# Kernel optimization log

Hardware: AMD Instinct MI355X
Metric: run time of the kernel (lower is better)

Reference implementation:

```python
import jax, jax.numpy as jnp
import numpy as np

N_LAYERS = 200
KSIZE = 7
L_IN = 1388
FC_IN = 188   # 1388 - 200*6
FC_OUT = 91


def setup_inputs() -> dict:
    key = jax.random.key(0)
    k_x, k_w, k_b, k_fw, k_fb = jax.random.split(key, 5)
    B = 1024
    x = jax.random.normal(k_x, (B, L_IN), dtype=jnp.float32)
    # Conv1d(1,1,7) weights: torch default init U(-s, s) with s = 1/sqrt(in_ch*k) = 1/sqrt(7)
    s = 1.0 / np.sqrt(KSIZE)
    conv_w = jax.random.uniform(k_w, (N_LAYERS, KSIZE), dtype=jnp.float32, minval=-s, maxval=s)
    conv_b = jax.random.uniform(k_b, (N_LAYERS,), dtype=jnp.float32, minval=-s, maxval=s)
    sf = 1.0 / np.sqrt(FC_IN)
    fc_w = jax.random.uniform(k_fw, (FC_OUT, FC_IN), dtype=jnp.float32, minval=-sf, maxval=sf)
    fc_b = jax.random.uniform(k_fb, (FC_OUT,), dtype=jnp.float32, minval=-sf, maxval=sf)
    return {"x": x, "conv_w": conv_w, "conv_b": conv_b, "fc_w": fc_w, "fc_b": fc_b}


def _conv1(h, w, b):
    # h: [B, L]; cross-correlation with taps w[0..6], valid padding -> [B, L-6]
    L_out = h.shape[1] - (KSIZE - 1)
    acc = w[0] * h[:, 0:L_out]
    for k in range(1, KSIZE):
        acc = acc + w[k] * h[:, k:k + L_out]
    return acc + b


def reference(x, conv_w, conv_b, fc_w, fc_b):
    h = x  # unsqueeze(1) is implicit: single channel handled as [B, L]
    for i in range(N_LAYERS):
        h = _conv1(h, conv_w[i], conv_b[i])
        if i < N_LAYERS - 1:  # last ReLU was popped in the torch module
            h = jax.nn.relu(h)
    # Linear(188, 91) applied to the length dim, then Sigmoid; squeeze channel dim
    out = jax.nn.sigmoid(h @ fc_w.T + fc_b)  # [B, 91]
    return out
```

## Files before the change

### kernel.cpp

```cpp
#include <hip/hip_runtime.h>
#include <math.h>

#define N_LAYERS 200
#define KSIZE 7
#define L_IN 1388
#define FC_IN 188
#define FC_OUT 91
#define NT 128
#define RMAX 12
#define NSTAGES 13

constexpr int s_lo(int s)  { return 16 * s; }
constexpr int s_hi(int s)  { return (s < 12) ? 16 * s + 16 : N_LAYERS; }
constexpr int lin_(int s)  { return L_IN - 6 * s_lo(s); }
constexpr int lout_(int s) { return L_IN - 6 * s_hi(s); }
constexpr int cut_(int s)  { return lout_(s) / 2; }
constexpr int marg_(int s) { return 6 * (s_hi(s) - s_lo(s)); }
constexpr int s_R(int s) {
    const int a = cut_(s) + marg_(s);
    const int b = lin_(s) - cut_(s);
    const int m = (a > b) ? a : b;
    return (m + 63) / 64;
}

__device__ __forceinline__ float dpp_next(float v) {
    return __int_as_float(
        __builtin_amdgcn_mov_dpp(__float_as_int(v), 0x130, 0xf, 0xf, true));
}

struct WG { float w[28]; float b[4]; };

__device__ __forceinline__ void load_wg(WG& wg, const float4* __restrict__ cw4,
                                        const float4* __restrict__ cb4, int g) {
#pragma unroll
    for (int t = 0; t < 7; ++t) {
        const float4 v = cw4[g * 7 + t];
        wg.w[4 * t + 0] = v.x; wg.w[4 * t + 1] = v.y;
        wg.w[4 * t + 2] = v.z; wg.w[4 * t + 3] = v.w;
    }
    const float4 bv = cb4[g];
    wg.b[0] = bv.x; wg.b[1] = bv.y; wg.b[2] = bv.z; wg.b[3] = bv.w;
}

template<int R, bool NR3>
__device__ __forceinline__ void run4(float (&r)[RMAX], const WG& wg) {
    constexpr int T1N = (R < 6) ? R : 6;
    constexpr int T2N = (R < 6) ? (6 - R) : 0;
#pragma unroll
    for (int j = 0; j < 4; ++j) {
        float t1[T1N];
#pragma unroll
        for (int t = 0; t < T1N; ++t) t1[t] = dpp_next(r[t]);
        float t2[T2N ? T2N : 1];
        if constexpr (T2N > 0) {
#pragma unroll
            for (int u = 0; u < T2N; ++u) t2[u] = dpp_next(t1[u]);
        }
        const bool relu = !(NR3 && j == 3);
#pragma unroll
        for (int k = 0; k < R; ++k) {
            float acc = wg.b[j];
#pragma unroll
            for (int d = 0; d < KSIZE; ++d) {
                const int m = k + d;
                const float v = (m < R) ? r[m]
                              : ((m - R < T1N) ? t1[m - R] : t2[m - 2 * R]);
                acc = fmaf(wg.w[j * 7 + d], v, acc);
            }
            r[k] = relu ? fmaxf(acc, 0.0f) : acc;
        }
    }
}

template<int R, bool FINAL>
__device__ __forceinline__ void run_stage_g(float (&r)[RMAX], WG& A,
        const float4* __restrict__ cw4, const float4* __restrict__ cb4,
        int g0, int g1) {
#pragma unroll 1
    for (int g = g0; g < g1; g += 2) {
        WG B;
        load_wg(B, cw4, cb4, (g + 1 < 50) ? g + 1 : 49);
        run4<R, false>(r, A);
        load_wg(A, cw4, cb4, (g + 2 < 50) ? g + 2 : 49);
        run4<R, FINAL>(r, B);
    }
}

template<int Ro, int Rn>
__device__ __forceinline__ void repack(float (&r)[RMAX], float* lbuf,
                                       int lane, int wid,
                                       int cut_o, int lout_o, int cut_n)
{
    const int base_o = wid ? cut_o : 0;
    const int bound  = wid ? lout_o : cut_o;
#pragma unroll
    for (int k = 0; k < Ro; ++k) {
        const int g = base_o + lane * Ro + k;
        if (g < bound) lbuf[g] = r[k];
    }
    __syncthreads();
    const int base_n = wid ? cut_n : 0;
#pragma unroll
    for (int k = 0; k < Rn; ++k) r[k] = lbuf[base_n + lane * Rn + k];
    __syncthreads();
}

template<int S>
struct Chain {
    __device__ static __forceinline__ void run(float (&r)[RMAX], WG& A,
        const float4* __restrict__ cw4, const float4* __restrict__ cb4,
        float* lbuf, int lane, int wid)
    {
        run_stage_g<s_R(S), false>(r, A, cw4, cb4, 4 * S, 4 * S + 4);
        repack<s_R(S), s_R(S + 1)>(r, lbuf, lane, wid,
                                   cut_(S), lout_(S), cut_(S + 1));
        Chain<S + 1>::run(r, A, cw4, cb4, lbuf, lane, wid);
    }
};

template<>
struct Chain<NSTAGES - 1> {
    __device__ static __forceinline__ void run(float (&r)[RMAX], WG& A,
        const float4* __restrict__ cw4, const float4* __restrict__ cb4,
        float* lbuf, int lane, int wid)
    {
        constexpr int R = s_R(NSTAGES - 1);
        run_stage_g<R, true>(r, A, cw4, cb4, 48, 50);
        const int base_o = wid ? 94 : 0;
        const int bound  = wid ? FC_IN : 94;
#pragma unroll
        for (int k = 0; k < R; ++k) {
            const int g = base_o + lane * R + k;
            if (g < bound) lbuf[g] = r[k];
        }
        __syncthreads();
    }
};

__global__ __launch_bounds__(NT) void conv_chain_kernel(
    const float* __restrict__ x,
    const float* __restrict__ conv_w,
    const float* __restrict__ conv_b,
    const float* __restrict__ fc_w,
    const float* __restrict__ fc_b,
    float* __restrict__ out)
{
    __shared__ __align__(16) float lbuf[1312];

    const int row  = blockIdx.x;
    const int tid  = threadIdx.x;
    const int lane = tid & 63;
    const int wid  = tid >> 6;

    const float4* cw4 = (const float4*)conv_w;
    const float4* cb4 = (const float4*)conv_b;

    WG A;
    load_wg(A, cw4, cb4, 0);

    float r[RMAX];
    const float* xr = x + (size_t)row * L_IN;
    constexpr int R0 = s_R(0);
    const int c0 = wid ? cut_(0) : 0;
#pragma unroll
    for (int k = 0; k < R0; ++k) {
        const int p = c0 + lane * R0 + k;
        r[k] = (p < L_IN) ? xr[p] : 0.0f;
    }

    Chain<0>::run(r, A, cw4, cb4, lbuf, lane, wid);

    if (tid < FC_OUT) {
        float acc = fc_b[tid];
        const float4* wp = (const float4*)(fc_w + tid * FC_IN);
        const float4* hp = (const float4*)lbuf;
#pragma unroll 4
        for (int q = 0; q < FC_IN / 4; ++q) {
            const float4 hv = hp[q];
            const float4 wv = wp[q];
            acc = fmaf(wv.x, hv.x, acc);
            acc = fmaf(wv.y, hv.y, acc);
            acc = fmaf(wv.z, hv.z, acc);
            acc = fmaf(wv.w, hv.w, acc);
        }
        out[(size_t)row * FC_OUT + tid] = 1.0f / (1.0f + expf(-acc));
    }
}

extern "C" void kernel_launch(void* const* d_in, const int* in_sizes, int n_in,
                              void* d_out, int out_size, void* d_ws, size_t ws_size,
                              hipStream_t stream) {
    const float* x      = (const float*)d_in[0];
    const float* conv_w = (const float*)d_in[1];
    const float* conv_b = (const float*)d_in[2];
    const float* fc_w   = (const float*)d_in[3];
    const float* fc_b   = (const float*)d_in[4];
    float* outp = (float*)d_out;

    const int batch = in_sizes[0] / L_IN;
    conv_chain_kernel<<<batch, NT, 0, stream>>>(x, conv_w, conv_b, fc_w, fc_b, outp);
}
```

Before: 120.0 us.

## Split each row across four wavefronts instead of two to shrink per-lane registers

```diff
diff --git a/kernel.cpp b/kernel.cpp
--- a/kernel.cpp
+++ b/kernel.cpp
@@ -6,21 +6,17 @@
 #define L_IN 1388
 #define FC_IN 188
 #define FC_OUT 91
-#define NT 128
-#define RMAX 12
+#define NT 256
+#define RMAX 7
 #define NSTAGES 13
 
-constexpr int s_lo(int s)  { return 16 * s; }
-constexpr int s_hi(int s)  { return (s < 12) ? 16 * s + 16 : N_LAYERS; }
-constexpr int lin_(int s)  { return L_IN - 6 * s_lo(s); }
-constexpr int lout_(int s) { return L_IN - 6 * s_hi(s); }
-constexpr int cut_(int s)  { return lout_(s) / 2; }
-constexpr int marg_(int s) { return 6 * (s_hi(s) - s_lo(s)); }
+constexpr int s_hi(int s)  { return (s < 12) ? 16 * (s + 1) : N_LAYERS; }
+constexpr int len_a(int s) { return L_IN - 6 * s_hi(s); }
+constexpr int q_(int s)    { return len_a(s) / 4; }
+constexpr int marg_(int s) { return (s < 12) ? 96 : 48; }
 constexpr int s_R(int s) {
-    const int a = cut_(s) + marg_(s);
-    const int b = lin_(s) - cut_(s);
-    const int m = (a > b) ? a : b;
-    return (m + 63) / 64;
+    const int r = (q_(s) + marg_(s) + 63) / 64;
+    return (r < 3) ? 3 : r;
 }
 
 __device__ __forceinline__ float dpp_next(float v) {
@@ -56,6 +52,7 @@
 #pragma unroll
             for (int u = 0; u < T2N; ++u) t2[u] = dpp_next(t1[u]);
         }
+
         const bool relu = !(NR3 && j == 3);
 #pragma unroll
         for (int k = 0; k < R; ++k) {
@@ -88,18 +85,17 @@
 
 template<int Ro, int Rn>
 __device__ __forceinline__ void repack(float (&r)[RMAX], float* lbuf,
-                                       int lane, int wid,
-                                       int cut_o, int lout_o, int cut_n)
+                                       int lane, int wid, int q_o, int q_n)
 {
-    const int base_o = wid ? cut_o : 0;
-    const int bound  = wid ? lout_o : cut_o;
+    const int base_o = wid * q_o;
+    const int bound  = base_o + q_o;
 #pragma unroll
     for (int k = 0; k < Ro; ++k) {
         const int g = base_o + lane * Ro + k;
         if (g < bound) lbuf[g] = r[k];
     }
     __syncthreads();
-    const int base_n = wid ? cut_n : 0;
+    const int base_n = wid * q_n;
 #pragma unroll
     for (int k = 0; k < Rn; ++k) r[k] = lbuf[base_n + lane * Rn + k];
     __syncthreads();
@@ -112,8 +108,7 @@
         float* lbuf, int lane, int wid)
     {
         run_stage_g<s_R(S), false>(r, A, cw4, cb4, 4 * S, 4 * S + 4);
-        repack<s_R(S), s_R(S + 1)>(r, lbuf, lane, wid,
-                                   cut_(S), lout_(S), cut_(S + 1));
+        repack<s_R(S), s_R(S + 1)>(r, lbuf, lane, wid, q_(S), q_(S + 1));
         Chain<S + 1>::run(r, A, cw4, cb4, lbuf, lane, wid);
     }
 };
@@ -126,8 +121,8 @@
     {
         constexpr int R = s_R(NSTAGES - 1);
         run_stage_g<R, true>(r, A, cw4, cb4, 48, 50);
-        const int base_o = wid ? 94 : 0;
-        const int bound  = wid ? FC_IN : 94;
+        const int base_o = wid * 47;
+        const int bound  = base_o + 47;
 #pragma unroll
         for (int k = 0; k < R; ++k) {
             const int g = base_o + lane * R + k;
@@ -137,7 +132,7 @@
     }
 };
 
-__global__ __launch_bounds__(NT) void conv_chain_kernel(
+__global__ __launch_bounds__(NT, 4) void conv_chain_kernel(
     const float* __restrict__ x,
     const float* __restrict__ conv_w,
     const float* __restrict__ conv_b,
@@ -145,7 +140,7 @@
     const float* __restrict__ fc_b,
     float* __restrict__ out)
 {
-    __shared__ __align__(16) float lbuf[1312];
+    __shared__ __align__(16) float lbuf[1352];
 
     const int row  = blockIdx.x;
     const int tid  = threadIdx.x;
@@ -161,7 +156,7 @@
     float r[RMAX];
     const float* xr = x + (size_t)row * L_IN;
     constexpr int R0 = s_R(0);
-    const int c0 = wid ? cut_(0) : 0;
+    const int c0 = wid * q_(0);
 #pragma unroll
     for (int k = 0; k < R0; ++k) {
         const int p = c0 + lane * R0 + k;
```

Result: slower. 130.3 us (+8.6%).
